# Performance work log

Hardware: AMD Instinct MI355X
Metric: run time of the kernel (lower is better)

The kernel has to match this reference:

```python
import jax, jax.numpy as jnp
import numpy as np

B, S, D, H = 2, 2048, 1024, 16
DK = D // H  # 64


def setup_inputs() -> dict:
    key = jax.random.key(0)
    ks = jax.random.split(key, 9)
    s = 0.02
    return {
        "embeddings": jax.random.normal(ks[0], (B, S, D), jnp.float32),
        "Wq": jax.random.normal(ks[1], (H, D, DK), jnp.float32) * s,
        "bq": jax.random.normal(ks[2], (H, DK), jnp.float32) * s,
        "Wk": jax.random.normal(ks[3], (H, D, DK), jnp.float32) * s,
        "bk": jax.random.normal(ks[4], (H, DK), jnp.float32) * s,
        "Wv": jax.random.normal(ks[5], (H, D, DK), jnp.float32) * s,
        "bv": jax.random.normal(ks[6], (H, DK), jnp.float32) * s,
        "Wo": jax.random.normal(ks[7], (D, D), jnp.float32) * s,
        "bo": jax.random.normal(ks[8], (D,), jnp.float32) * s,
    }


def reference(embeddings, Wq, bq, Wk, bk, Wv, bv, Wo, bo):
    b, s, d = embeddings.shape
    dk = Wq.shape[-1]
    # batched per-head projections: [b,s,d] x [h,d,k] -> [b,h,s,k]
    q = jnp.einsum('bsd,hdk->bhsk', embeddings, Wq) + bq[None, :, None, :]
    k = jnp.einsum('bsd,hdk->bhsk', embeddings, Wk) + bk[None, :, None, :]
    v = jnp.einsum('bsd,hdk->bhsk', embeddings, Wv) + bv[None, :, None, :]
    scores = jnp.einsum('bhqk,bhsk->bhqs', q, k) / jnp.sqrt(jnp.float32(dk))
    causal_mask = jnp.triu(jnp.ones((s, s), dtype=bool), k=1)  # True above diagonal
    scores = jnp.where(causal_mask, jnp.float32(-1e9), scores)
    weights = jax.nn.softmax(scores, axis=-1)
    ctx = jnp.einsum('bhqs,bhsk->bhqk', weights, v)
    concat = ctx.transpose(0, 2, 1, 3).reshape(b, s, d)  # head-major concat, matches torch.cat
    return concat @ Wo + bo
```

## Files before the change

kernel.cpp:

```cpp
#include <hip/hip_runtime.h>
#include <hip/hip_bf16.h>

typedef unsigned short u16;
typedef unsigned int u32;
typedef __bf16 bf16x8 __attribute__((ext_vector_type(8)));
typedef float f32x4 __attribute__((ext_vector_type(4)));
typedef float f32x16 __attribute__((ext_vector_type(16)));

#define AS1 __attribute__((address_space(1)))
#define AS3 __attribute__((address_space(3)))

#define NB 2
#define NS 2048
#define ND 1024
#define NH 16
#define NK 64

__device__ __forceinline__ u16 f2bf(float f) {
  u32 u = __builtin_bit_cast(u32, f);
  return (u16)((u + 0x7FFFu + ((u >> 16) & 1u)) >> 16);
}

__device__ __forceinline__ u32 cvt_pk_bf16(float lo, float hi) {
  u32 u;
  asm("v_cvt_pk_bf16_f32 %0, %1, %2" : "=v"(u) : "v"(lo), "v"(hi));
  return u;
}

__device__ __forceinline__ void stage_tile(u16* lds, const u16* __restrict__ src, int rs,
                                           int wid, int lane) {
#pragma unroll
  for (int i = 0; i < 2; ++i) {
    int c = wid * 128 + i * 64 + lane;
    int row = c >> 3;
    int kc = (c & 7) ^ (row & 7);
    __builtin_amdgcn_global_load_lds((const AS1 u32*)(src + (size_t)row * rs + kc * 8),
                                     (AS3 u32*)(lds + (wid * 128 + i * 64) * 8), 16, 0, 0);
  }
}

__device__ __forceinline__ void stage_tile2(u16* lds, const u16* __restrict__ src, int rs,
                                            int w, int lane) {
#pragma unroll
  for (int i = 0; i < 4; ++i) {
    int c = w * 256 + i * 64 + lane;
    int row = c >> 3;
    int kc = (c & 7) ^ (row & 7);
    __builtin_amdgcn_global_load_lds((const AS1 u32*)(src + (size_t)row * rs + kc * 8),
                                     (AS3 u32*)(lds + (w * 256 + i * 64) * 8), 16, 0, 0);
  }
}

__device__ __forceinline__ bf16x8 read_slot(const u16* lds, int row, int slot) {
  return *(const bf16x8*)(lds + row * 64 + (slot ^ (row & 7)) * 8);
}

__device__ __forceinline__ uint2 ld8(const u16* lds, int row, int col) {
  int slot = (col >> 3) ^ (row & 7);
  return *(const uint2*)(lds + row * 64 + slot * 8 + (col & 7));
}

__device__ __forceinline__ bf16x8 read_vfrag(const u16* lds, int row, int ks, int hi) {
  int c0 = ks * 16 + 4 * hi;
  uint2 a = ld8(lds, row, c0);
  uint2 b = ld8(lds, row, c0 + 8);
  uint4 q; q.x = a.x; q.y = a.y; q.z = b.x; q.w = b.y;
  return __builtin_bit_cast(bf16x8, q);
}

__device__ __forceinline__ bf16x8 read_frag(const u16* lds, int row, int ks, int lane) {
  int slot = ((lane >> 4) + ks * 4) ^ (row & 7);
  return *(const bf16x8*)(lds + row * 64 + slot * 8);
}

__global__ __launch_bounds__(256) void convert_kernel(const float* __restrict__ src,
                                                      u16* __restrict__ dst, int n) {
  int i = (blockIdx.x * 256 + threadIdx.x) * 4;
  if (i >= n) return;
  float4 v = *(const float4*)(src + i);
  u32 w0 = cvt_pk_bf16(v.x, v.y);
  u32 w1 = cvt_pk_bf16(v.z, v.w);
  uint2 w; w.x = w0; w.y = w1;
  *(uint2*)(dst + i) = w;
}

__global__ __launch_bounds__(256) void transpose_conv(const float* __restrict__ src,
                                                      u16* __restrict__ dst, int R, int C) {
  __shared__ float tile[32][33];
  size_t base = (size_t)blockIdx.z * R * C;
  src += base;
  dst += base;
  int c0 = blockIdx.x * 32, r0 = blockIdx.y * 32;
  int tx = threadIdx.x, ty = threadIdx.y;
#pragma unroll
  for (int i = 0; i < 4; ++i)
    tile[ty + 8 * i][tx] = src[(size_t)(r0 + ty + 8 * i) * C + c0 + tx];
  __syncthreads();
#pragma unroll
  for (int i = 0; i < 4; ++i)
    dst[(size_t)(c0 + ty + 8 * i) * R + r0 + tx] = f2bf(tile[tx][ty + 8 * i]);
}

template <int MODE>
__global__ __launch_bounds__(256) void gemm128(const u16* __restrict__ A,
                                               const u16* __restrict__ Bt,
                                               const float* __restrict__ b0,
                                               const float* __restrict__ b1,
                                               const float* __restrict__ b2,
                                               u16* __restrict__ Qo, u16* __restrict__ Ko,
                                               u16* __restrict__ Vo,
                                               float* __restrict__ out) {
  __shared__ alignas(16) u16 lds_a[128 * 64];
  __shared__ alignas(16) u16 lds_b[128 * 64];
  int tid = threadIdx.x, lane = tid & 63, wid = tid >> 6;
  int wm = wid >> 1, wn = wid & 1;
  int m0 = blockIdx.x * 128, n0 = blockIdx.y * 128;
  int col = lane & 15;
  f32x4 zero4 = {0.f, 0.f, 0.f, 0.f};
  f32x4 acc[4][4];
#pragma unroll
  for (int i = 0; i < 4; ++i)
#pragma unroll
    for (int j = 0; j < 4; ++j) acc[i][j] = zero4;
  for (int k0 = 0; k0 < ND; k0 += 64) {
    stage_tile(lds_a, A + (size_t)m0 * ND + k0, ND, wid, lane);
    stage_tile(lds_a + 4096, A + (size_t)(m0 + 64) * ND + k0, ND, wid, lane);
    stage_tile(lds_b, Bt + (size_t)n0 * ND + k0, ND, wid, lane);
    stage_tile(lds_b + 4096, Bt + (size_t)(n0 + 64) * ND + k0, ND, wid, lane);
    __syncthreads();
#pragma unroll
    for (int ks = 0; ks < 2; ++ks) {
      bf16x8 af[4], bf[4];
#pragma unroll
      for (int i = 0; i < 4; ++i) af[i] = read_frag(lds_a, wm * 64 + i * 16 + col, ks, lane);
#pragma unroll
      for (int j = 0; j < 4; ++j) bf[j] = read_frag(lds_b, wn * 64 + j * 16 + col, ks, lane);
#pragma unroll
      for (int i = 0; i < 4; ++i)
#pragma unroll
        for (int j = 0; j < 4; ++j)
          acc[i][j] = __builtin_amdgcn_mfma_f32_16x16x32_bf16(af[i], bf[j], acc[i][j], 0, 0, 0);
    }
    __syncthreads();
  }
  int rbase = m0 + wm * 64 + (lane >> 4) * 4;
#pragma unroll
  for (int j = 0; j < 4; ++j) {
    int n = n0 + wn * 64 + j * 16 + col;
    if constexpr (MODE == 0) {
      int which = n >> 10, hh = (n >> 6) & 15, dk = n & 63;
      const float* bp = which == 0 ? b0 : which == 1 ? b1 : b2;
      float bn = bp[hh * 64 + dk];
      if (which == 0) {
#pragma unroll
        for (int i = 0; i < 4; ++i)
#pragma unroll
          for (int r = 0; r < 4; ++r) {
            int m = rbase + i * 16 + r;
            int bb = m >> 11, s = m & (NS - 1);
            Qo[((size_t)(bb * NH + hh) * NS + s) * NK + dk] =
                f2bf((acc[i][j][r] + bn) * 0.18033688f);
          }
      } else if (which == 1) {
#pragma unroll
        for (int i = 0; i < 4; ++i)
#pragma unroll
          for (int r = 0; r < 4; ++r) {
            int m = rbase + i * 16 + r;
            int bb = m >> 11, s = m & (NS - 1);
            Ko[((size_t)(bb * NH + hh) * NS + s) * NK + dk] = f2bf(acc[i][j][r] + bn);
          }
      } else {
#pragma unroll
        for (int i = 0; i < 4; ++i)
#pragma unroll
          for (int r = 0; r < 4; ++r) {
            int m = rbase + i * 16 + r;
            int bb = m >> 11, s = m & (NS - 1);
            Vo[((size_t)(bb * NH + hh) * NK + dk) * NS + s] = f2bf(acc[i][j][r] + bn);
          }
      }
    } else {
      float bn = b0[n];
#pragma unroll
      for (int i = 0; i < 4; ++i)
#pragma unroll
        for (int r = 0; r < 4; ++r)
          out[(size_t)(rbase + i * 16 + r) * ND + n] = acc[i][j][r] + bn;
    }
  }
}

__global__ __launch_bounds__(128, 2) void attn_kernel(const u16* __restrict__ Q,
                                                      const u16* __restrict__ K,
                                                      const u16* __restrict__ Vt,
                                                      u16* __restrict__ ctx) {
  __shared__ alignas(16) u16 lds_k[2][64 * 64];
  __shared__ alignas(16) u16 lds_v[2][64 * 64];
  __shared__ float slab[2][32];
  int tid = threadIdx.x, lane = tid & 63, w = tid >> 6;
  int hi = lane >> 5, ln = lane & 31;
  int bh = blockIdx.x;
  int pr = blockIdx.y;
  const u16* Qb = Q + bh * (NS * NK);
  const u16* Kb = K + bh * (NS * NK);
  const u16* Vb = Vt + bh * (NK * NS);
  int b = bh >> 4, h = bh & 15;

#pragma unroll 1
  for (int half = 0; half < 2; ++half) {
    int qt = half ? pr : (31 - pr);
    int q0w = qt * 64 + w * 32;
    int qg = q0w + ln;
    bf16x8 qf[4];
#pragma unroll
    for (int ks = 0; ks < 4; ++ks)
      qf[ks] = *(const bf16x8*)(Qb + qg * NK + ks * 16 + hi * 8);

    f32x16 acc0, acc1;
#pragma unroll
    for (int r = 0; r < 16; ++r) { acc0[r] = 0.f; acc1[r] = 0.f; }
    float lp = 0.f;
    int nt = qt + 1;

    stage_tile2(lds_k[0], Kb, NK, w, lane);
    stage_tile2(lds_v[0], Vb, NS, w, lane);
    __syncthreads();

    for (int t = 0; t < nt; ++t) {
      int cur = t & 1;
      if (t + 1 < nt) {
        stage_tile2(lds_k[cur ^ 1], Kb + (t + 1) * 64 * NK, NK, w, lane);
        stage_tile2(lds_v[cur ^ 1], Vb + (t + 1) * 64, NS, w, lane);
      }
      const u16* lk = lds_k[cur];
      const u16* lv = lds_v[cur];
      f32x16 sc0, sc1;
#pragma unroll
      for (int r = 0; r < 16; ++r) { sc0[r] = 0.f; sc1[r] = 0.f; }
      __builtin_amdgcn_s_setprio(1);
#pragma unroll
      for (int ks = 0; ks < 4; ++ks) {
        bf16x8 kf0 = read_slot(lk, ln, 2 * ks + hi);
        sc0 = __builtin_amdgcn_mfma_f32_32x32x16_bf16(kf0, qf[ks], sc0, 0, 0, 0);
        bf16x8 kf1 = read_slot(lk, 32 + ln, 2 * ks + hi);
        sc1 = __builtin_amdgcn_mfma_f32_32x32x16_bf16(kf1, qf[ks], sc1, 0, 0, 0);
      }
      __builtin_amdgcn_s_setprio(0);
      if (t == qt) {
#pragma unroll
        for (int r = 0; r < 16; ++r) {
          int kl = t * 64 + (r & 3) + 8 * (r >> 2) + 4 * hi;
          if (kl > qg) sc0[r] = -1e30f;
          if (kl + 32 > qg) sc1[r] = -1e30f;
        }
      }
      float ps[4] = {0.f, 0.f, 0.f, 0.f};
#pragma unroll
      for (int r = 0; r < 16; ++r) {
        float p = exp2f(sc0[r]);
        sc0[r] = p;
        ps[r & 3] += p;
      }
#pragma unroll
      for (int r = 0; r < 16; ++r) {
        float p = exp2f(sc1[r]);
        sc1[r] = p;
        ps[r & 3] += p;
      }
      lp += (ps[0] + ps[1]) + (ps[2] + ps[3]);
      u32 wd[8];
      bf16x8 pa[4];
#pragma unroll
      for (int i = 0; i < 8; ++i) wd[i] = cvt_pk_bf16(sc0[2 * i], sc0[2 * i + 1]);
      { uint4 q4; q4.x = wd[0]; q4.y = wd[1]; q4.z = wd[2]; q4.w = wd[3];
        pa[0] = __builtin_bit_cast(bf16x8, q4);
        q4.x = wd[4]; q4.y = wd[5]; q4.z = wd[6]; q4.w = wd[7];
        pa[1] = __builtin_bit_cast(bf16x8, q4); }
#pragma unroll
      for (int i = 0; i < 8; ++i) wd[i] = cvt_pk_bf16(sc1[2 * i], sc1[2 * i + 1]);
      { uint4 q4; q4.x = wd[0]; q4.y = wd[1]; q4.z = wd[2]; q4.w = wd[3];
        pa[2] = __builtin_bit_cast(bf16x8, q4);
        q4.x = wd[4]; q4.y = wd[5]; q4.z = wd[6]; q4.w = wd[7];
        pa[3] = __builtin_bit_cast(bf16x8, q4); }
      __builtin_amdgcn_s_setprio(1);
#pragma unroll
      for (int ks = 0; ks < 4; ++ks) {
        bf16x8 vf0 = read_vfrag(lv, ln, ks, hi);
        acc0 = __builtin_amdgcn_mfma_f32_32x32x16_bf16(pa[ks], vf0, acc0, 0, 0, 0);
        bf16x8 vf1 = read_vfrag(lv, 32 + ln, ks, hi);
        acc1 = __builtin_amdgcn_mfma_f32_32x32x16_bf16(pa[ks], vf1, acc1, 0, 0, 0);
      }
      __builtin_amdgcn_s_setprio(0);
      __syncthreads();
    }
    lp += __shfl_xor(lp, 32);
    if (!hi) slab[w][ln] = 1.0f / lp;
    float iv[16];
#pragma unroll
    for (int r = 0; r < 16; ++r) iv[r] = slab[w][(r & 3) + 8 * (r >> 2) + 4 * hi];
#pragma unroll
    for (int r = 0; r < 16; ++r) {
      int qq = q0w + (r & 3) + 8 * (r >> 2) + 4 * hi;
      size_t base = (size_t)(b * NS + qq) * ND + h * NK + ln;
      ctx[base] = f2bf(acc0[r] * iv[r]);
      ctx[base + 32] = f2bf(acc1[r] * iv[r]);
    }
  }
}

extern "C" void kernel_launch(void* const* d_in, const int* in_sizes, int n_in,
                              void* d_out, int out_size, void* d_ws, size_t ws_size,
                              hipStream_t stream) {
  (void)in_sizes; (void)n_in; (void)out_size;
  const float* emb = (const float*)d_in[0];
  const float* Wq = (const float*)d_in[1];
  const float* bq = (const float*)d_in[2];
  const float* Wk = (const float*)d_in[3];
  const float* bk = (const float*)d_in[4];
  const float* Wv = (const float*)d_in[5];
  const float* bv = (const float*)d_in[6];
  const float* Wo = (const float*)d_in[7];
  const float* bo = (const float*)d_in[8];
  float* out = (float*)d_out;

  const size_t EMB_N = (size_t)NB * NS * ND;
  const size_t W_N = (size_t)NH * ND * NK;
  const size_t QKV_N = (size_t)NB * NH * NS * NK;
  if (ws_size < (EMB_N + 4 * W_N + 3 * QKV_N) * sizeof(u16)) return;
  u16* ws = (u16*)d_ws;
  u16* emb_bf = ws;
  u16* Wqt = emb_bf + EMB_N;
  u16* Wkt = Wqt + W_N;
  u16* Wvt = Wkt + W_N;
  u16* Wot = Wvt + W_N;
  u16* Qb = Wot + W_N;
  u16* Kb = Qb + QKV_N;
  u16* Vtb = Kb + QKV_N;
  u16* ctxb = emb_bf;

  convert_kernel<<<dim3((int)(EMB_N / 4 / 256)), dim3(256), 0, stream>>>(emb, emb_bf,
                                                                         (int)EMB_N);
  dim3 tb(32, 8);
  transpose_conv<<<dim3(2, 32, 16), tb, 0, stream>>>(Wq, Wqt, ND, NK);
  transpose_conv<<<dim3(2, 32, 16), tb, 0, stream>>>(Wk, Wkt, ND, NK);
  transpose_conv<<<dim3(2, 32, 16), tb, 0, stream>>>(Wv, Wvt, ND, NK);
  transpose_conv<<<dim3(32, 32, 1), tb, 0, stream>>>(Wo, Wot, ND, ND);
  gemm128<0><<<dim3(32, 24), dim3(256), 0, stream>>>(emb_bf, Wqt, bq, bk, bv, Qb, Kb, Vtb,
                                                     nullptr);
  attn_kernel<<<dim3(32, 16), dim3(128), 0, stream>>>(Qb, Kb, Vtb, ctxb);
  gemm128<1><<<dim3(32, 8), dim3(256), 0, stream>>>(ctxb, Wot, bo, nullptr, nullptr,
                                                    nullptr, nullptr, nullptr, out);
}
```

Measured before the change: 147.5 us.

## Give each warp private K/V LDS buffers with vmcnt waits instead of block barriers

The attention kernel stops sharing K/V tiles across its two warps. Each warp now stages full 64x64 K and V tiles into its own double-buffered LDS region and prefetches two tiles ahead, using s_waitcnt vmcnt counters in place of __syncthreads. The V-projection epilogue writes s in a permuted order so V fragments can be read with one 16-byte swizzled read_slot instead of two 8-byte reads. This removes per-tile block barriers and cheapens the V fragment loads, at the cost of twice the global load traffic per block and double the LDS footprint, which may reduce occupancy.

```diff
diff --git a/kernel.cpp b/kernel.cpp
--- a/kernel.cpp
+++ b/kernel.cpp
@@ -39,33 +39,20 @@
   }
 }
 
-__device__ __forceinline__ void stage_tile2(u16* lds, const u16* __restrict__ src, int rs,
-                                            int w, int lane) {
-#pragma unroll
-  for (int i = 0; i < 4; ++i) {
-    int c = w * 256 + i * 64 + lane;
+__device__ __forceinline__ void stage_warp(u16* lds, const u16* __restrict__ src, int rs,
+                                           int lane) {
+#pragma unroll
+  for (int i = 0; i < 8; ++i) {
+    int c = i * 64 + lane;
     int row = c >> 3;
     int kc = (c & 7) ^ (row & 7);
     __builtin_amdgcn_global_load_lds((const AS1 u32*)(src + (size_t)row * rs + kc * 8),
-                                     (AS3 u32*)(lds + (w * 256 + i * 64) * 8), 16, 0, 0);
+                                     (AS3 u32*)(lds + i * 512), 16, 0, 0);
   }
 }
 
 __device__ __forceinline__ bf16x8 read_slot(const u16* lds, int row, int slot) {
   return *(const bf16x8*)(lds + row * 64 + (slot ^ (row & 7)) * 8);
-}
-
-__device__ __forceinline__ uint2 ld8(const u16* lds, int row, int col) {
-  int slot = (col >> 3) ^ (row & 7);
-  return *(const uint2*)(lds + row * 64 + slot * 8 + (col & 7));
-}
-
-__device__ __forceinline__ bf16x8 read_vfrag(const u16* lds, int row, int ks, int hi) {
-  int c0 = ks * 16 + 4 * hi;
-  uint2 a = ld8(lds, row, c0);
-  uint2 b = ld8(lds, row, c0 + 8);
-  uint4 q; q.x = a.x; q.y = a.y; q.z = b.x; q.w = b.y;
-  return __builtin_bit_cast(bf16x8, q);
 }
 
 __device__ __forceinline__ bf16x8 read_frag(const u16* lds, int row, int ks, int lane) {
@@ -177,7 +164,8 @@
           for (int r = 0; r < 4; ++r) {
             int m = rbase + i * 16 + r;
             int bb = m >> 11, s = m & (NS - 1);
-            Vo[((size_t)(bb * NH + hh) * NK + dk) * NS + s] = f2bf(acc[i][j][r] + bn);
+            int ss = (s & ~12) | ((s & 4) << 1) | ((s & 8) >> 1);
+            Vo[((size_t)(bb * NH + hh) * NK + dk) * NS + ss] = f2bf(acc[i][j][r] + bn);
           }
       }
     } else {
@@ -195,8 +183,7 @@
                                                       const u16* __restrict__ K,
                                                       const u16* __restrict__ Vt,
                                                       u16* __restrict__ ctx) {
-  __shared__ alignas(16) u16 lds_k[2][64 * 64];
-  __shared__ alignas(16) u16 lds_v[2][64 * 64];
+  __shared__ alignas(16) u16 lds[2][2][8192];
   __shared__ float slab[2][32];
   int tid = threadIdx.x, lane = tid & 63, w = tid >> 6;
   int hi = lane >> 5, ln = lane & 31;
@@ -206,6 +193,10 @@
   const u16* Kb = K + bh * (NS * NK);
   const u16* Vb = Vt + bh * (NK * NS);
   int b = bh >> 4, h = bh & 15;
+  u16* myK0 = &lds[w][0][0];
+  u16* myV0 = &lds[w][0][4096];
+  u16* myK1 = &lds[w][1][0];
+  u16* myV1 = &lds[w][1][4096];
 
 #pragma unroll 1
   for (int half = 0; half < 2; ++half) {
@@ -223,18 +214,23 @@
     float lp = 0.f;
     int nt = qt + 1;
 
-    stage_tile2(lds_k[0], Kb, NK, w, lane);
-    stage_tile2(lds_v[0], Vb, NS, w, lane);
-    __syncthreads();
-
+    stage_warp(myK0, Kb, NK, lane);
+    stage_warp(myV0, Vb, NS, lane);
+    if (nt > 1) {
+      stage_warp(myK1, Kb + 64 * NK, NK, lane);
+      stage_warp(myV1, Vb + 64, NS, lane);
+    }
+
+#pragma unroll 1
     for (int t = 0; t < nt; ++t) {
-      int cur = t & 1;
+      const u16* lk = (t & 1) ? myK1 : myK0;
+      const u16* lv = (t & 1) ? myV1 : myV0;
       if (t + 1 < nt) {
-        stage_tile2(lds_k[cur ^ 1], Kb + (t + 1) * 64 * NK, NK, w, lane);
-        stage_tile2(lds_v[cur ^ 1], Vb + (t + 1) * 64, NS, w, lane);
-      }
-      const u16* lk = lds_k[cur];
-      const u16* lv = lds_v[cur];
+        asm volatile("s_waitcnt vmcnt(16)" ::: "memory");
+      } else {
+        asm volatile("s_waitcnt vmcnt(0)" ::: "memory");
+      }
+      __builtin_amdgcn_sched_barrier(0);
       f32x16 sc0, sc1;
 #pragma unroll
       for (int r = 0; r < 16; ++r) { sc0[r] = 0.f; sc1[r] = 0.f; }
@@ -286,13 +282,20 @@
       __builtin_amdgcn_s_setprio(1);
 #pragma unroll
       for (int ks = 0; ks < 4; ++ks) {
-        bf16x8 vf0 = read_vfrag(lv, ln, ks, hi);
+        bf16x8 vf0 = read_slot(lv, ln, 2 * ks + hi);
         acc0 = __builtin_amdgcn_mfma_f32_32x32x16_bf16(pa[ks], vf0, acc0, 0, 0, 0);
-        bf16x8 vf1 = read_vfrag(lv, 32 + ln, ks, hi);
+        bf16x8 vf1 = read_slot(lv, 32 + ln, 2 * ks + hi);
         acc1 = __builtin_amdgcn_mfma_f32_32x32x16_bf16(pa[ks], vf1, acc1, 0, 0, 0);
       }
       __builtin_amdgcn_s_setprio(0);
-      __syncthreads();
+      if (t + 2 < nt) {
+        asm volatile("s_waitcnt lgkmcnt(0)" ::: "memory");
+        __builtin_amdgcn_sched_barrier(0);
+        u16* nk = (t & 1) ? myK1 : myK0;
+        u16* nv = (t & 1) ? myV1 : myV0;
+        stage_warp(nk, Kb + (t + 2) * 64 * NK, NK, lane);
+        stage_warp(nv, Vb + (t + 2) * 64, NS, lane);
+      }
     }
     lp += __shfl_xor(lp, 32);
     if (!hi) slab[w][ln] = 1.0f / lp;
```

New measurement: 141.6 us. 1.04x faster.
